# Kernel tuning notes

Measured on AMD Instinct MI355X. Metric: run time of the kernel, lower is better.

Reference implementation:

```python
import jax, jax.numpy as jnp
import numpy as np

B, C, D, H, W = 2, 96, 32, 64, 64
NH = 3
WS = (4, 4, 4)
SS = (2, 2, 2)
N = WS[0] * WS[1] * WS[2]
HD = C // NH
SCALE = HD ** -0.5

def _rel_pos_index():
    cd, ch, cw = np.meshgrid(np.arange(WS[0]), np.arange(WS[1]), np.arange(WS[2]), indexing='ij')
    coords = np.stack([cd, ch, cw]).reshape(3, -1)  # [3, N]
    rel = (coords[:, :, None] - coords[:, None, :]).transpose(1, 2, 0)  # [N, N, 3]
    rel[:, :, 0] += WS[0] - 1
    rel[:, :, 1] += WS[1] - 1
    rel[:, :, 2] += WS[2] - 1
    rel[:, :, 0] *= (2 * WS[1] - 1) * (2 * WS[2] - 1)
    rel[:, :, 1] *= 2 * WS[2] - 1
    return rel.sum(-1)  # [N, N]

REL_IDX = jnp.asarray(_rel_pos_index().reshape(-1))

def _win_part_np(x):
    b, d, h, w, c = x.shape
    x = x.reshape(b, d // WS[0], WS[0], h // WS[1], WS[1], w // WS[2], WS[2], c)
    return x.transpose(0, 1, 3, 5, 2, 4, 6, 7).reshape(-1, N, c)

def _attn_mask():
    img = np.zeros((1, D, H, W, 1), np.float32)
    cnt = 0
    for ds in (slice(-WS[0]), slice(-WS[0], -SS[0]), slice(-SS[0], None)):
        for hs in (slice(-WS[1]), slice(-WS[1], -SS[1]), slice(-SS[1], None)):
            for ws in (slice(-WS[2]), slice(-WS[2], -SS[2]), slice(-SS[2], None)):
                img[:, ds, hs, ws, :] = cnt
                cnt += 1
    mw = _win_part_np(img)[:, :, 0]  # [nW, N]
    diff = mw[:, None, :] - mw[:, :, None]
    return jnp.asarray(np.where(diff != 0, -100.0, 0.0).astype(np.float32))

ATTN_MASK = _attn_mask()  # [nW, N, N]

def _ln(x, g, b):
    mu = x.mean(-1, keepdims=True)
    var = ((x - mu) ** 2).mean(-1, keepdims=True)
    return (x - mu) * jax.lax.rsqrt(var + 1e-5) * g + b

def _win_part(x):
    b, d, h, w, c = x.shape
    x = x.reshape(b, d // WS[0], WS[0], h // WS[1], WS[1], w // WS[2], WS[2], c)
    return jnp.transpose(x, (0, 1, 3, 5, 2, 4, 6, 7)).reshape(-1, N, c)

def _win_rev(wins, b, d, h, w):
    x = wins.reshape(b, d // WS[0], h // WS[1], w // WS[2], WS[0], WS[1], WS[2], -1)
    return jnp.transpose(x, (0, 1, 4, 2, 5, 3, 6, 7)).reshape(b, d, h, w, -1)

def _block(x, n1g, n1b, qw, qb, rpb, pw, pb, n2g, n2b, f1w, f1b, f2w, f2b, shifted):
    b, d, h, w, c = x.shape
    shortcut = x
    xn = _ln(x, n1g, n1b)
    if shifted:
        xn = jnp.roll(xn, (-SS[0], -SS[1], -SS[2]), axis=(1, 2, 3))
    xw = _win_part(xn)  # [Bw, N, C]
    bw = xw.shape[0]
    qkv = (xw @ qw.T + qb).reshape(bw, N, 3, NH, HD)
    qkv = jnp.transpose(qkv, (2, 0, 3, 1, 4))
    q, k, v = qkv[0], qkv[1], qkv[2]  # [Bw, NH, N, HD]
    attn = jnp.einsum('bhnd,bhmd->bhnm', q * SCALE, k)
    bias = rpb[REL_IDX].reshape(N, N, NH).transpose(2, 0, 1)  # [NH, N, N]
    attn = attn + bias[None]
    if shifted:
        nw = ATTN_MASK.shape[0]
        attn = (attn.reshape(bw // nw, nw, NH, N, N) + ATTN_MASK[None, :, None]).reshape(bw, NH, N, N)
    attn = jax.nn.softmax(attn, axis=-1)
    out = jnp.einsum('bhnm,bhmd->bnhd', attn, v).reshape(bw, N, c)
    out = out @ pw.T + pb
    out = _win_rev(out, b, d, h, w)
    if shifted:
        out = jnp.roll(out, SS, axis=(1, 2, 3))
    x = shortcut + out
    xn = _ln(x, n2g, n2b)
    hid = jax.nn.gelu(xn @ f1w.T + f1b, approximate=False)
    return x + (hid @ f2w.T + f2b)

def setup_inputs() -> dict:
    key = jax.random.key(0)
    ks = jax.random.split(key, 8)
    T = (2 * WS[0] - 1) * (2 * WS[1] - 1) * (2 * WS[2] - 1)
    p = lambda k, shape, s=0.02: jax.random.normal(k, shape, jnp.float32) * s
    return {
        'x': jax.random.normal(ks[0], (B, C, D, H, W), jnp.float32),
        'norm1_g': jnp.ones((2, C), jnp.float32), 'norm1_b': jnp.zeros((2, C), jnp.float32),
        'qkv_w': p(ks[1], (2, 3 * C, C)), 'qkv_b': jnp.zeros((2, 3 * C), jnp.float32),
        'rpb': p(ks[2], (2, T, NH)),
        'proj_w': p(ks[3], (2, C, C)), 'proj_b': jnp.zeros((2, C), jnp.float32),
        'norm2_g': jnp.ones((2, C), jnp.float32), 'norm2_b': jnp.zeros((2, C), jnp.float32),
        'fc1_w': p(ks[4], (2, 4 * C, C)), 'fc1_b': jnp.zeros((2, 4 * C), jnp.float32),
        'fc2_w': p(ks[5], (2, C, 4 * C)), 'fc2_b': jnp.zeros((2, C), jnp.float32),
    }

def reference(x, norm1_g, norm1_b, qkv_w, qkv_b, rpb, proj_w, proj_b, norm2_g, norm2_b, fc1_w, fc1_b, fc2_w, fc2_b):
    x = jnp.transpose(x, (0, 2, 3, 4, 1))  # b d h w c
    for i in range(2):
        x = _block(x, norm1_g[i], norm1_b[i], qkv_w[i], qkv_b[i], rpb[i], proj_w[i], proj_b[i],
                   norm2_g[i], norm2_b[i], fc1_w[i], fc1_b[i], fc2_w[i], fc2_b[i], shifted=(i == 1))
    return jnp.transpose(x, (0, 4, 1, 2, 3))
```

## Files before the change

kernel.cpp:

```cpp
#include <hip/hip_runtime.h>
#include <math.h>

typedef unsigned short u16;
typedef unsigned int u32;
#define DEVI __device__ __forceinline__

typedef __attribute__((ext_vector_type(8))) short bf16x8;
typedef __attribute__((ext_vector_type(4))) float f32x4;

constexpr int kB = 2, kC = 96, kD = 32, kH = 64, kW = 64;
constexpr int kS = kD * kH * kW;
constexpr int kM = kB * kS;
constexpr float kScale = 0.17677669529663687f;

DEVI u16 f2bf(float f) {
  u32 x = __float_as_uint(f);
  return (u16)((x + 0x7fffu + ((x >> 16) & 1u)) >> 16);
}
DEVI float bf2f(u16 v) { return __uint_as_float(((u32)v) << 16); }
DEVI u32 pack2(float a, float b) { return (u32)f2bf(a) | ((u32)f2bf(b) << 16); }

DEVI float gelu_f(float v) {
  float x = v * 0.70710678118654752f;
  float ax = fabsf(x);
  float t = __builtin_amdgcn_rcpf(fmaf(0.3275911f, ax, 1.0f));
  float y = t * fmaf(t, fmaf(t, fmaf(t, fmaf(t, 1.061405429f, -1.453152027f),
                                     1.421413741f), -0.284496736f), 0.254829592f);
  float e = __expf(-x * x);
  float erfv = copysignf(fmaf(-y, e, 1.0f), x);
  return 0.5f * v * (1.0f + erfv);
}

__global__ void k_tin(const float* __restrict__ in, float* __restrict__ out) {
  __shared__ float tile[32][33];
  int s0 = blockIdx.x << 5, c0 = blockIdx.y << 5, b = blockIdx.z;
  int tx = threadIdx.x, ty = threadIdx.y;
#pragma unroll
  for (int q = 0; q < 4; q++)
    tile[ty + q * 8][tx] = in[((size_t)(b * kC + c0 + ty + q * 8)) * kS + s0 + tx];
  __syncthreads();
#pragma unroll
  for (int q = 0; q < 4; q++)
    out[((size_t)(b * kS + s0 + ty + q * 8)) * kC + c0 + tx] = tile[tx][ty + q * 8];
}

__global__ void k_tout(const float* __restrict__ in, float* __restrict__ out) {
  __shared__ float tile[32][33];
  int s0 = blockIdx.x << 5, c0 = blockIdx.y << 5, b = blockIdx.z;
  int tx = threadIdx.x, ty = threadIdx.y;
#pragma unroll
  for (int q = 0; q < 4; q++)
    tile[ty + q * 8][tx] = in[((size_t)(b * kS + s0 + ty + q * 8)) * kC + c0 + tx];
  __syncthreads();
#pragma unroll
  for (int q = 0; q < 4; q++)
    out[((size_t)(b * kC + c0 + ty + q * 8)) * kS + s0 + tx] = tile[tx][ty + q * 8];
}

__global__ __launch_bounds__(256) void k_wcvt(const float* __restrict__ q,
                                              const float* __restrict__ p,
                                              const float* __restrict__ f1,
                                              const float* __restrict__ f2,
                                              u16* dq, u16* dp, u16* df1, u16* df2) {
  int a = blockIdx.y;
  const float* sp; u16* dst; int n;
  if (a == 0)      { sp = q;  dst = dq;  n = 2 * 288 * 96; }
  else if (a == 1) { sp = p;  dst = dp;  n = 2 * 96 * 96; }
  else if (a == 2) { sp = f1; dst = df1; n = 2 * 384 * 96; }
  else             { sp = f2; dst = df2; n = 2 * 96 * 384; }
  for (int i = (blockIdx.x * 256 + threadIdx.x) * 4; i < n; i += gridDim.x * 1024) {
    float4 v = *(const float4*)(sp + i);
    *(u32*)(dst + i) = pack2(v.x, v.y);
    *(u32*)(dst + i + 2) = pack2(v.z, v.w);
  }
}

__global__ __launch_bounds__(1024, 4) void k_qa(const float* __restrict__ BX,
                                                const float* __restrict__ g1,
                                                const float* __restrict__ be1,
                                                const u16* __restrict__ Wq,
                                                const float* __restrict__ bq,
                                                const float* __restrict__ rpb,
                                                u16* __restrict__ out, int shifted) {
  __shared__ __align__(16) char arena[70720];
  u16* QK = (u16*)arena;
  u16* VT = (u16*)(arena + 51200);
  float* RP = (float*)(arena + 66560);

  int tid = threadIdx.x, wv = tid >> 6, lane = tid & 63;
  int llo = lane & 15, lhi = lane >> 4;
  int r0 = blockIdx.x << 7;
  int rowb = (wv >> 1) * 16;
  int colb = (wv & 1) * 48;

  for (int t = tid; t < 1029; t += 1024) {
    int head = t / 343, idx = t - head * 343;
    RP[t] = rpb[idx * 3 + head];
  }

  {
    int r = r0 + rowb + llo;
    int wI = r >> 6, n = r & 63;
    int Xw = wI & 15, Xh = (wI >> 4) & 15, Xd = (wI >> 8) & 7, Xb = wI >> 11;
    int d = Xd * 4 + (n >> 4), h = Xh * 4 + ((n >> 2) & 3), w = Xw * 4 + (n & 3);
    if (shifted) { d = (d + 2) & 31; h = (h + 2) & 63; w = (w + 2) & 63; }
    const float* xr = BX + (size_t)(((Xb * kD + d) * kH + h) * kW + w) * 96;
    float xv[3][8];
#pragma unroll
    for (int ks = 0; ks < 3; ks++) {
      float4 p0 = *(const float4*)(xr + ks * 32 + lhi * 8);
      float4 p1 = *(const float4*)(xr + ks * 32 + lhi * 8 + 4);
      xv[ks][0] = p0.x; xv[ks][1] = p0.y; xv[ks][2] = p0.z; xv[ks][3] = p0.w;
      xv[ks][4] = p1.x; xv[ks][5] = p1.y; xv[ks][6] = p1.z; xv[ks][7] = p1.w;
    }
    float sum = 0.f;
#pragma unroll
    for (int ks = 0; ks < 3; ks++)
#pragma unroll
      for (int e = 0; e < 8; e++) sum += xv[ks][e];
    sum += __shfl_xor(sum, 16); sum += __shfl_xor(sum, 32);
    float mean = sum * (1.f / 96.f);
    float vs = 0.f;
#pragma unroll
    for (int ks = 0; ks < 3; ks++)
#pragma unroll
      for (int e = 0; e < 8; e++) { float dd = xv[ks][e] - mean; vs += dd * dd; }
    vs += __shfl_xor(vs, 16); vs += __shfl_xor(vs, 32);
    float rstd = rsqrtf(vs * (1.f / 96.f) + 1e-5f);
    bf16x8 a[3];
#pragma unroll
    for (int ks = 0; ks < 3; ks++) {
      const float* gp = g1 + ks * 32 + lhi * 8;
      const float* bp = be1 + ks * 32 + lhi * 8;
      float4 g0 = *(const float4*)gp, g4 = *(const float4*)(gp + 4);
      float4 b0 = *(const float4*)bp, b4 = *(const float4*)(bp + 4);
      float gf[8] = {g0.x, g0.y, g0.z, g0.w, g4.x, g4.y, g4.z, g4.w};
      float bf[8] = {b0.x, b0.y, b0.z, b0.w, b4.x, b4.y, b4.z, b4.w};
      bf16x8 t;
#pragma unroll
      for (int e = 0; e < 8; e++)
        t[e] = (short)f2bf((xv[ks][e] - mean) * rstd * gf[e] + bf[e]);
      a[ks] = t;
    }

    for (int c = 0; c < 3; c++) {
      f32x4 acc[3];
#pragma unroll
      for (int j = 0; j < 3; j++) acc[j] = (f32x4){0.f, 0.f, 0.f, 0.f};
#pragma unroll
      for (int ks = 0; ks < 3; ks++)
#pragma unroll
        for (int j = 0; j < 3; j++) {
          bf16x8 b = *(const bf16x8*)(Wq + (size_t)(c * 96 + colb + j * 16 + llo) * 96 +
                                      ks * 32 + lhi * 8);
          acc[j] = __builtin_amdgcn_mfma_f32_16x16x32_bf16(a[ks], b, acc[j], 0, 0, 0);
        }
      if (c < 2) {
#pragma unroll
        for (int j = 0; j < 3; j++) {
          int col = colb + j * 16 + llo;
          float bb_ = bq[c * 96 + col];
#pragma unroll
          for (int rg = 0; rg < 4; rg++)
            QK[(rowb + lhi * 4 + rg) * 200 + c * 96 + col] = f2bf(acc[j][rg] + bb_);
        }
      } else {
#pragma unroll
        for (int j = 0; j < 3; j++) {
          int dcol = colb + j * 16 + llo;
          float bb_ = bq[192 + dcol];
          int head = dcol >> 5, dd = dcol & 31;
#pragma unroll
          for (int rg = 0; rg < 4; rg++) {
            int row = rowb + lhi * 4 + rg;
            VT[(((row >> 6) * 3 + head) * 32 + dd) * 40 + (row & 63)] = f2bf(acc[j][rg] + bb_);
          }
        }
      }
    }
  }
  __syncthreads();

  int u = wv;
  bool active = (u < 12);
  int pair = u / 6, rem = u - pair * 6, head = rem >> 1, qh = rem & 1;
  int widx = (blockIdx.x << 1) + pair;
  int ww = widx & 15, wh = (widx >> 4) & 15, wd = (widx >> 8) & 7;
  const float* rp = RP + head * 343;
  const u16* qkw = QK + pair * 64 * 200;
  u16* plw = QK + u * 2112;

  f32x4 s[2][4];
  bf16x8 bv[2][2];
  if (active) {
    bf16x8 aq[2], bk[4];
#pragma unroll
    for (int qt2 = 0; qt2 < 2; qt2++)
      aq[qt2] = *(const bf16x8*)&qkw[(qh * 32 + qt2 * 16 + llo) * 200 + head * 32 + lhi * 8];
#pragma unroll
    for (int kt = 0; kt < 4; kt++)
      bk[kt] = *(const bf16x8*)&qkw[(kt * 16 + llo) * 200 + 96 + head * 32 + lhi * 8];
    const u16* vtb = VT + (pair * 3 + head) * 32 * 40;
#pragma unroll
    for (int jt = 0; jt < 2; jt++)
#pragma unroll
      for (int ks = 0; ks < 2; ks++)
        bv[jt][ks] = *(const bf16x8*)&vtb[(jt * 16 + llo) * 40 + ks * 32 + lhi * 8];

#pragma unroll
    for (int qt2 = 0; qt2 < 2; qt2++)
#pragma unroll
      for (int kt = 0; kt < 4; kt++)
        s[qt2][kt] = __builtin_amdgcn_mfma_f32_16x16x32_bf16(
            aq[qt2], bk[kt], (f32x4){0.f, 0.f, 0.f, 0.f}, 0, 0, 0);

    int jh = llo >> 2, jw = llo & 3;
    int mi_h = (wh == 15) ? (1 + (lhi >= 2)) : 0;
    int mj_hw = ((wh == 15) ? (1 + (jh >= 2)) : 0) * 3 +
                ((ww == 15) ? (1 + (jw >= 2)) : 0);
#pragma unroll
    for (int qt2 = 0; qt2 < 2; qt2++) {
      int qt = qh * 2 + qt2;
#pragma unroll
      for (int kt = 0; kt < 4; kt++) {
        const float* rb = &rp[(qt - kt + 3) * 49 + (lhi - jh + 3) * 7 + (3 - jw)];
#pragma unroll
        for (int e = 0; e < 4; e++) {
          float val = fmaf(s[qt2][kt][e], kScale, rb[e]);
          if (shifted) {
            int ci = ((wd == 7) ? (1 + (qt >= 2)) : 0) * 9 + mi_h * 3 +
                     ((ww == 15) ? (1 + (e >= 2)) : 0);
            int cj = ((wd == 7) ? (1 + (kt >= 2)) : 0) * 9 + mj_hw;
            if (ci != cj) val -= 100.f;
          }
          s[qt2][kt][e] = val;
        }
      }
    }
#pragma unroll
    for (int qt2 = 0; qt2 < 2; qt2++) {
      f32x4 m;
#pragma unroll
      for (int e = 0; e < 4; e++)
        m[e] = fmaxf(fmaxf(s[qt2][0][e], s[qt2][1][e]), fmaxf(s[qt2][2][e], s[qt2][3][e]));
#pragma unroll
      for (int msk = 1; msk <= 8; msk <<= 1)
#pragma unroll
        for (int e = 0; e < 4; e++) m[e] = fmaxf(m[e], __shfl_xor(m[e], msk));
      f32x4 sum2 = (f32x4){0.f, 0.f, 0.f, 0.f};
#pragma unroll
      for (int kt = 0; kt < 4; kt++)
#pragma unroll
        for (int e = 0; e < 4; e++) {
          float p = __expf(s[qt2][kt][e] - m[e]);
          s[qt2][kt][e] = p;
          sum2[e] += p;
        }
#pragma unroll
      for (int msk = 1; msk <= 8; msk <<= 1)
#pragma unroll
        for (int e = 0; e < 4; e++) sum2[e] += __shfl_xor(sum2[e], msk);
#pragma unroll
      for (int e = 0; e < 4; e++) sum2[e] = 1.f / sum2[e];
#pragma unroll
      for (int kt = 0; kt < 4; kt++)
#pragma unroll
        for (int e = 0; e < 4; e++) s[qt2][kt][e] *= sum2[e];
    }
  }
  __syncthreads();
  if (active) {
#pragma unroll
    for (int qt2 = 0; qt2 < 2; qt2++)
#pragma unroll
      for (int kt = 0; kt < 4; kt++)
#pragma unroll
        for (int e = 0; e < 4; e++)
          plw[(qt2 * 16 + lhi * 4 + e) * 66 + kt * 16 + llo] = f2bf(s[qt2][kt][e]);
  }
  __syncthreads();
  if (active) {
    f32x4 o[2][2];
#pragma unroll
    for (int qt2 = 0; qt2 < 2; qt2++) {
      o[qt2][0] = (f32x4){0.f, 0.f, 0.f, 0.f};
      o[qt2][1] = (f32x4){0.f, 0.f, 0.f, 0.f};
#pragma unroll
      for (int ks = 0; ks < 2; ks++) {
        bf16x8 pa = *(const bf16x8*)&plw[(qt2 * 16 + llo) * 66 + ks * 32 + lhi * 8];
        o[qt2][0] = __builtin_amdgcn_mfma_f32_16x16x32_bf16(pa, bv[0][ks], o[qt2][0], 0, 0, 0);
        o[qt2][1] = __builtin_amdgcn_mfma_f32_16x16x32_bf16(pa, bv[1][ks], o[qt2][1], 0, 0, 0);
      }
    }
    u16* ob = out + (size_t)widx * 64 * 96 + head * 32;
#pragma unroll
    for (int qt2 = 0; qt2 < 2; qt2++)
#pragma unroll
      for (int jt = 0; jt < 2; jt++)
#pragma unroll
        for (int e = 0; e < 4; e++)
          ob[(size_t)(qh * 32 + qt2 * 16 + lhi * 4 + e) * 96 + jt * 16 + llo] =
              f2bf(o[qt2][jt][e]);
  }
}

__global__ __launch_bounds__(256, 2) void k_pm(const u16* __restrict__ X,
                                               const u16* __restrict__ Wp,
                                               const float* __restrict__ bp,
                                               const float* __restrict__ lng,
                                               const float* __restrict__ lnb,
                                               const u16* __restrict__ W1,
                                               const float* __restrict__ b1,
                                               const u16* __restrict__ W2,
                                               const float* __restrict__ b2,
                                               float* __restrict__ bx, int shifted) {
  __shared__ __align__(16) u16 Xs[128 * 104];
  __shared__ __align__(16) u16 Hs[128 * 104];
  int tid = threadIdx.x;
  int wv = tid >> 6, lane = tid & 63;
  int llo = lane & 15, lhi = lane >> 4;
  int r0 = blockIdx.x << 7;
  int rowb = wv * 32;

  float vv[2][4][6];
#pragma unroll
  for (int i = 0; i < 2; i++)
#pragma unroll
    for (int rg = 0; rg < 4; rg++) {
      int row = r0 + rowb + i * 16 + lhi * 4 + rg;
#pragma unroll
      for (int j = 0; j < 6; j++)
        vv[i][rg][j] = bx[(size_t)row * 96 + j * 16 + llo];
    }

  bf16x8 a[2][3];
#pragma unroll
  for (int i = 0; i < 2; i++) {
    int r = r0 + rowb + i * 16 + llo;
    int w = r & 63, h = (r >> 6) & 63, d = (r >> 12) & 31, bb = r >> 17;
    if (shifted) { d = (d + 30) & 31; h = (h + 62) & 63; w = (w + 62) & 63; }
    int widx = ((bb * 8 + (d >> 2)) * 16 + (h >> 2)) * 16 + (w >> 2);
    int rsrc = (widx << 6) + ((d & 3) << 4) + ((h & 3) << 2) + (w & 3);
#pragma unroll
    for (int ks = 0; ks < 3; ks++)
      a[i][ks] = *(const bf16x8*)(X + (size_t)rsrc * 96 + ks * 32 + lhi * 8);
  }

  {
    f32x4 acc[2][6];
#pragma unroll
    for (int i = 0; i < 2; i++)
#pragma unroll
      for (int j = 0; j < 6; j++) acc[i][j] = (f32x4){0.f, 0.f, 0.f, 0.f};
#pragma unroll
    for (int ks = 0; ks < 3; ks++) {
      bf16x8 b[6];
#pragma unroll
      for (int j = 0; j < 6; j++)
        b[j] = *(const bf16x8*)(Wp + (size_t)(j * 16 + llo) * 96 + ks * 32 + lhi * 8);
#pragma unroll
      for (int i = 0; i < 2; i++)
#pragma unroll
        for (int j = 0; j < 6; j++)
          acc[i][j] = __builtin_amdgcn_mfma_f32_16x16x32_bf16(a[i][ks], b[j], acc[i][j], 0, 0, 0);
    }

    float bj[6], gj[6], betaj[6];
#pragma unroll
    for (int j = 0; j < 6; j++) {
      int col = j * 16 + llo;
      bj[j] = bp[col]; gj[j] = lng[col]; betaj[j] = lnb[col];
    }
#pragma unroll
    for (int i = 0; i < 2; i++) {
#pragma unroll
      for (int rg = 0; rg < 4; rg++) {
        int lrow = rowb + i * 16 + lhi * 4 + rg;
        float sum = 0.f;
#pragma unroll
        for (int j = 0; j < 6; j++) {
          vv[i][rg][j] += acc[i][j][rg] + bj[j];
          sum += vv[i][rg][j];
        }
#pragma unroll
        for (int m = 1; m <= 8; m <<= 1) sum += __shfl_xor(sum, m);
        float mean = sum * (1.f / 96.f);
        float vs = 0.f;
#pragma unroll
        for (int j = 0; j < 6; j++) { float dd = vv[i][rg][j] - mean; vs += dd * dd; }
#pragma unroll
        for (int m = 1; m <= 8; m <<= 1) vs += __shfl_xor(vs, m);
        float rstd = rsqrtf(vs * (1.f / 96.f) + 1e-5f);
#pragma unroll
        for (int j = 0; j < 6; j++)
          Xs[lrow * 104 + j * 16 + llo] =
              f2bf((vv[i][rg][j] - mean) * rstd * gj[j] + betaj[j]);
      }
    }
  }

  bf16x8 ax[2][3];
#pragma unroll
  for (int i = 0; i < 2; i++)
#pragma unroll
    for (int ks = 0; ks < 3; ks++)
      ax[i][ks] = *(const bf16x8*)&Xs[(rowb + i * 16 + llo) * 104 + ks * 32 + lhi * 8];

  f32x4 acc2[2][6];
#pragma unroll
  for (int i = 0; i < 2; i++)
#pragma unroll
    for (int j = 0; j < 6; j++) acc2[i][j] = (f32x4){0.f, 0.f, 0.f, 0.f};

  for (int c = 0; c < 4; c++) {
    f32x4 acc[2][6];
#pragma unroll
    for (int i = 0; i < 2; i++)
#pragma unroll
      for (int j = 0; j < 6; j++) acc[i][j] = (f32x4){0.f, 0.f, 0.f, 0.f};
#pragma unroll
    for (int ks = 0; ks < 3; ks++)
#pragma unroll
      for (int j = 0; j < 6; j++) {
        bf16x8 b = *(const bf16x8*)(W1 + (size_t)(c * 96 + j * 16 + llo) * 96 +
                                    ks * 32 + lhi * 8);
        acc[0][j] = __builtin_amdgcn_mfma_f32_16x16x32_bf16(ax[0][ks], b, acc[0][j], 0, 0, 0);
        acc[1][j] = __builtin_amdgcn_mfma_f32_16x16x32_bf16(ax[1][ks], b, acc[1][j], 0, 0, 0);
      }
#pragma unroll
    for (int j = 0; j < 6; j++) {
      float bb_ = b1[c * 96 + j * 16 + llo];
#pragma unroll
      for (int i = 0; i < 2; i++)
#pragma unroll
        for (int rg = 0; rg < 4; rg++)
          Hs[(rowb + i * 16 + lhi * 4 + rg) * 104 + j * 16 + llo] =
              f2bf(gelu_f(acc[i][j][rg] + bb_));
    }
    bf16x8 ah[2][3];
#pragma unroll
    for (int i = 0; i < 2; i++)
#pragma unroll
      for (int ks = 0; ks < 3; ks++)
        ah[i][ks] = *(const bf16x8*)&Hs[(rowb + i * 16 + llo) * 104 + ks * 32 + lhi * 8];
#pragma unroll
    for (int ks = 0; ks < 3; ks++)
#pragma unroll
      for (int j = 0; j < 6; j++) {
        bf16x8 b = *(const bf16x8*)(W2 + (size_t)(j * 16 + llo) * 384 + c * 96 +
                                    ks * 32 + lhi * 8);
        acc2[0][j] = __builtin_amdgcn_mfma_f32_16x16x32_bf16(ah[0][ks], b, acc2[0][j], 0, 0, 0);
        acc2[1][j] = __builtin_amdgcn_mfma_f32_16x16x32_bf16(ah[1][ks], b, acc2[1][j], 0, 0, 0);
      }
  }

#pragma unroll
  for (int i = 0; i < 2; i++)
#pragma unroll
    for (int j = 0; j < 6; j++) {
      float bb_ = b2[j * 16 + llo];
#pragma unroll
      for (int rg = 0; rg < 4; rg++) {
        size_t off = (size_t)(r0 + rowb + i * 16 + lhi * 4 + rg) * 96 + j * 16 + llo;
        bx[off] = vv[i][rg][j] + acc2[i][j][rg] + bb_;
      }
    }
}

extern "C" void kernel_launch(void* const* d_in, const int* in_sizes, int n_in,
                              void* d_out, int out_size, void* d_ws, size_t ws_size,
                              hipStream_t stream) {
  const float* x_in = (const float*)d_in[0];
  const float* n1g = (const float*)d_in[1];
  const float* n1b = (const float*)d_in[2];
  const float* qkvw = (const float*)d_in[3];
  const float* qkvb = (const float*)d_in[4];
  const float* rpb = (const float*)d_in[5];
  const float* projw = (const float*)d_in[6];
  const float* projb = (const float*)d_in[7];
  const float* n2g = (const float*)d_in[8];
  const float* n2b = (const float*)d_in[9];
  const float* fc1w = (const float*)d_in[10];
  const float* fc1b = (const float*)d_in[11];
  const float* fc2w = (const float*)d_in[12];
  const float* fc2b = (const float*)d_in[13];
  float* outp = (float*)d_out;

  char* ws = (char*)d_ws;
  float* bx = (float*)ws;
  u16* bb = (u16*)(ws + 100663296);
  u16* wq_bf = (u16*)(ws + 150994944);
  u16* wp_bf = wq_bf + 2 * 288 * 96;
  u16* w1_bf = wp_bf + 2 * 96 * 96;
  u16* w2_bf = w1_bf + 2 * 384 * 96;

  k_tin<<<dim3(kS / 32, 3, kB), dim3(32, 8), 0, stream>>>(x_in, bx);
  k_wcvt<<<dim3(72, 4), 256, 0, stream>>>(qkvw, projw, fc1w, fc2w,
                                          wq_bf, wp_bf, w1_bf, w2_bf);

  for (int blk = 0; blk < 2; blk++) {
    int sh = blk;
    k_qa<<<kM / 128, 1024, 0, stream>>>(bx, n1g + blk * 96, n1b + blk * 96,
                                        wq_bf + blk * 288 * 96, qkvb + blk * 288,
                                        rpb + blk * 343 * 3, bb, sh);
    k_pm<<<kM / 128, 256, 0, stream>>>(bb, wp_bf + blk * 96 * 96, projb + blk * 96,
                                       n2g + blk * 96, n2b + blk * 96,
                                       w1_bf + blk * 384 * 96, fc1b + blk * 384,
                                       w2_bf + blk * 96 * 384, fc2b + blk * 96,
                                       bx, sh);
  }

  k_tout<<<dim3(kS / 32, 3, kB), dim3(32, 8), 0, stream>>>(bx, outp);
}
```

Before: 728.0 us.

## Fuse output transpose into final MLP kernel and share LDS arena

Removes the separate k_tout transpose by having the second block's k_pm template variant stage results in shared memory and write directly in channel-major output layout. The Xs/Hs buffers are overlaid in a single arena and launch bounds are raised to 3 blocks per SM, with barriers added so the reuse is safe. This saves one full read and write pass over the activation tensor plus a launch. In exchange it adds block-wide barriers in the MLP loop and puts more pressure on registers.

```diff
diff --git a/kernel.cpp b/kernel.cpp
--- a/kernel.cpp
+++ b/kernel.cpp
@@ -42,19 +42,6 @@
 #pragma unroll
   for (int q = 0; q < 4; q++)
     out[((size_t)(b * kS + s0 + ty + q * 8)) * kC + c0 + tx] = tile[tx][ty + q * 8];
-}
-
-__global__ void k_tout(const float* __restrict__ in, float* __restrict__ out) {
-  __shared__ float tile[32][33];
-  int s0 = blockIdx.x << 5, c0 = blockIdx.y << 5, b = blockIdx.z;
-  int tx = threadIdx.x, ty = threadIdx.y;
-#pragma unroll
-  for (int q = 0; q < 4; q++)
-    tile[ty + q * 8][tx] = in[((size_t)(b * kS + s0 + ty + q * 8)) * kC + c0 + tx];
-  __syncthreads();
-#pragma unroll
-  for (int q = 0; q < 4; q++)
-    out[((size_t)(b * kC + c0 + ty + q * 8)) * kS + s0 + tx] = tile[tx][ty + q * 8];
 }
 
 __global__ __launch_bounds__(256) void k_wcvt(const float* __restrict__ q,
@@ -304,7 +291,8 @@
   }
 }
 
-__global__ __launch_bounds__(256, 2) void k_pm(const u16* __restrict__ X,
+template <int TOUT>
+__global__ __launch_bounds__(256, 3) void k_pm(const u16* __restrict__ X,
                                                const u16* __restrict__ Wp,
                                                const float* __restrict__ bp,
                                                const float* __restrict__ lng,
@@ -313,11 +301,14 @@
                                                const float* __restrict__ b1,
                                                const u16* __restrict__ W2,
                                                const float* __restrict__ b2,
-                                               float* __restrict__ bx, int shifted) {
-  __shared__ __align__(16) u16 Xs[128 * 104];
-  __shared__ __align__(16) u16 Hs[128 * 104];
-  int tid = threadIdx.x;
-  int wv = tid >> 6, lane = tid & 63;
+                                               float* __restrict__ bx,
+                                               float* __restrict__ outd, int shifted) {
+  __shared__ __align__(16) char arena[53248];
+  u16* Xs = (u16*)arena;
+  u16* Hs = (u16*)(arena + 26624);
+  float* Lo = (float*)arena;
+
+  int tid = threadIdx.x, wv = tid >> 6, lane = tid & 63;
   int llo = lane & 15, lhi = lane >> 4;
   int r0 = blockIdx.x << 7;
   int rowb = wv * 32;
@@ -398,6 +389,7 @@
       }
     }
   }
+  __syncthreads();
 
   bf16x8 ax[2][3];
 #pragma unroll
@@ -437,6 +429,7 @@
           Hs[(rowb + i * 16 + lhi * 4 + rg) * 104 + j * 16 + llo] =
               f2bf(gelu_f(acc[i][j][rg] + bb_));
     }
+    __syncthreads();
     bf16x8 ah[2][3];
 #pragma unroll
     for (int i = 0; i < 2; i++)
@@ -452,19 +445,43 @@
         acc2[0][j] = __builtin_amdgcn_mfma_f32_16x16x32_bf16(ah[0][ks], b, acc2[0][j], 0, 0, 0);
         acc2[1][j] = __builtin_amdgcn_mfma_f32_16x16x32_bf16(ah[1][ks], b, acc2[1][j], 0, 0, 0);
       }
-  }
-
-#pragma unroll
-  for (int i = 0; i < 2; i++)
-#pragma unroll
-    for (int j = 0; j < 6; j++) {
-      float bb_ = b2[j * 16 + llo];
-#pragma unroll
-      for (int rg = 0; rg < 4; rg++) {
-        size_t off = (size_t)(r0 + rowb + i * 16 + lhi * 4 + rg) * 96 + j * 16 + llo;
-        bx[off] = vv[i][rg][j] + acc2[i][j][rg] + bb_;
-      }
-    }
+    __syncthreads();
+  }
+
+  if (TOUT == 0) {
+#pragma unroll
+    for (int i = 0; i < 2; i++)
+#pragma unroll
+      for (int j = 0; j < 6; j++) {
+        float bb_ = b2[j * 16 + llo];
+#pragma unroll
+        for (int rg = 0; rg < 4; rg++) {
+          size_t off = (size_t)(r0 + rowb + i * 16 + lhi * 4 + rg) * 96 + j * 16 + llo;
+          bx[off] = vv[i][rg][j] + acc2[i][j][rg] + bb_;
+        }
+      }
+  } else {
+    float* LoW = Lo + wv * 32 * 98;
+#pragma unroll
+    for (int i = 0; i < 2; i++)
+#pragma unroll
+      for (int j = 0; j < 6; j++) {
+        float bb_ = b2[j * 16 + llo];
+#pragma unroll
+        for (int rg = 0; rg < 4; rg++)
+          LoW[(i * 16 + lhi * 4 + rg) * 98 + j * 16 + llo] =
+              vv[i][rg][j] + acc2[i][j][rg] + bb_;
+      }
+    __syncthreads();
+    int b = r0 >> 17;
+    int sbase = (r0 + rowb) & (kS - 1);
+    int ss = lane & 31, ch = lane >> 5;
+#pragma unroll
+    for (int c2 = 0; c2 < 48; c2++) {
+      int c = c2 * 2 + ch;
+      outd[((size_t)(b * kC + c)) * kS + sbase + ss] = LoW[ss * 98 + c];
+    }
+  }
 }
 
 extern "C" void kernel_launch(void* const* d_in, const int* in_sizes, int n_in,
@@ -498,17 +515,14 @@
   k_wcvt<<<dim3(72, 4), 256, 0, stream>>>(qkvw, projw, fc1w, fc2w,
                                           wq_bf, wp_bf, w1_bf, w2_bf);
 
-  for (int blk = 0; blk < 2; blk++) {
-    int sh = blk;
-    k_qa<<<kM / 128, 1024, 0, stream>>>(bx, n1g + blk * 96, n1b + blk * 96,
-                                        wq_bf + blk * 288 * 96, qkvb + blk * 288,
-                                        rpb + blk * 343 * 3, bb, sh);
-    k_pm<<<kM / 128, 256, 0, stream>>>(bb, wp_bf + blk * 96 * 96, projb + blk * 96,
-                                       n2g + blk * 96, n2b + blk * 96,
-                                       w1_bf + blk * 384 * 96, fc1b + blk * 384,
-                                       w2_bf + blk * 96 * 384, fc2b + blk * 96,
-                                       bx, sh);
-  }
-
-  k_tout<<<dim3(kS / 32, 3, kB), dim3(32, 8), 0, stream>>>(bx, outp);
-}
+  k_qa<<<kM / 128, 1024, 0, stream>>>(bx, n1g, n1b, wq_bf, qkvb,
+                                      rpb, bb, 0);
+  k_pm<0><<<kM / 128, 256, 0, stream>>>(bb, wp_bf, projb, n2g, n2b,
+                                        w1_bf, fc1b, w2_bf, fc2b, bx, nullptr, 0);
+  k_qa<<<kM / 128, 1024, 0, stream>>>(bx, n1g + 96, n1b + 96, wq_bf + 288 * 96,
+                                      qkvb + 288, rpb + 343 * 3, bb, 1);
+  k_pm<1><<<kM / 128, 256, 0, stream>>>(bb, wp_bf + 96 * 96, projb + 96,
+                                        n2g + 96, n2b + 96, w1_bf + 384 * 96,
+                                        fc1b + 384, w2_bf + 96 * 384, fc2b + 96,
+                                        bx, outp, 1);
+}
```

Result: faster. 684.8 us (median of 2 runs) (-5.9%).
